# Kernel tuning notes

Hardware: AMD Instinct MI355X
Metric: run time of the kernel (lower is better)

Reference implementation:

```python
import jax, jax.numpy as jnp
import numpy as np

N_NODES = 10000
N_EDGES = 160000
IN_CH = 256
HIDDEN = 512
N_LAYERS = 2
W_SCALE = 0.05  # keep relu chain numerically tame


def setup_inputs() -> dict:
    key = jax.random.key(0)
    ks = jax.random.split(key, 8)
    x = jax.random.normal(ks[0], (N_NODES, IN_CH), dtype=jnp.float32)
    edge_index = jax.random.randint(ks[1], (2, N_EDGES), 0, N_NODES, dtype=jnp.int64)
    W_in = jax.random.normal(ks[2], (IN_CH, HIDDEN), dtype=jnp.float32) * W_SCALE
    b_in = jnp.zeros((HIDDEN,), jnp.float32)
    msg_W = jax.random.normal(ks[3], (N_LAYERS, HIDDEN, HIDDEN), dtype=jnp.float32) * W_SCALE
    msg_b = jnp.zeros((N_LAYERS, HIDDEN), jnp.float32)
    upd_W = jax.random.normal(ks[4], (N_LAYERS, 2 * HIDDEN, HIDDEN), dtype=jnp.float32) * W_SCALE
    upd_b = jnp.zeros((N_LAYERS, HIDDEN), jnp.float32)
    W_out = jax.random.normal(ks[5], (HIDDEN, 1), dtype=jnp.float32) * W_SCALE
    b_out = jnp.zeros((1,), jnp.float32)
    return {"x": x, "edge_index": edge_index, "W_in": W_in, "b_in": b_in,
            "msg_W": msg_W, "msg_b": msg_b, "upd_W": upd_W, "upd_b": upd_b,
            "W_out": W_out, "b_out": b_out}


def reference(x, edge_index, W_in, b_in, msg_W, msg_b, upd_W, upd_b, W_out, b_out):
    src = edge_index[0]  # x_j source nodes (PyG source_to_target flow)
    dst = edge_index[1]  # aggregate into destination nodes
    n = x.shape[0]
    h = jax.nn.relu(x @ W_in + b_in)  # [N, H]
    for l in range(msg_W.shape[0]):
        # message: relu(Linear(x_j)) on gathered source features  [E, H]
        m = jax.nn.relu(h[src] @ msg_W[l] + msg_b[l])
        # aggr='add': scatter-add over destination nodes  [N, H]
        aggr = jax.ops.segment_sum(m, dst, num_segments=n)
        # update: relu(Linear(concat([x, aggr])))  [N, H]
        h = jax.nn.relu(jnp.concatenate([h, aggr], axis=-1) @ upd_W[l] + upd_b[l])
    out = h @ W_out + b_out  # [N, 1]
    return out.squeeze(-1)
```

## Files before the change

### kernel.cpp

```cpp
#include <hip/hip_runtime.h>


typedef _Float16 half8 __attribute__((ext_vector_type(8)));
typedef float float4v __attribute__((ext_vector_type(4)));

#define ASYNC_COPY16(gptr, lptr)                                              \
    __builtin_amdgcn_global_load_lds(                                         \
        (const __attribute__((address_space(1))) void*)(gptr),                \
        (__attribute__((address_space(3))) void*)(lptr), 16, 0, 0)


__device__ __forceinline__ void gemm_body(int id,
    const _Float16* __restrict__ A1, int KT1,
    const _Float16* __restrict__ A2, int KT2,
    const _Float16* __restrict__ Wt, int KTw, int ktw2,
    const float* __restrict__ bias, _Float16* __restrict__ C,
    int M, int Mtiles, int packC, int do_relu,
    const float* __restrict__ Wout, const float* __restrict__ bout,
    float* __restrict__ outp)
{
    __shared__ _Float16 As[4096];
    __shared__ _Float16 Bs[4096];

    const int tid  = threadIdx.x;
    const int wave = tid >> 6, lane = tid & 63;

    const int cxcd = id & 7, j = id >> 3;
    const int mt = cxcd + 8 * (j >> 3);
    if (mt >= Mtiles) return;
    const int pn = j & 7;
    const int bm = mt * 64, bn = pn * 64;

    const int wr = (wave >> 1) * 32, wc = (wave & 1) * 32;
    const int m16 = lane & 15, quad = lane >> 4;

    float4v acc[2][2] = {};
    float bv[2];
    #pragma unroll
    for (int jj = 0; jj < 2; ++jj) bv[jj] = bias[bn + wc + jj * 16 + m16];

    for (int pass = 0; pass < 2; ++pass) {
        const _Float16* __restrict__ A = pass ? A2 : A1;
        if (A == nullptr) continue;
        const int KTa  = pass ? KT2 : KT1;
        const int ktw0 = pass ? ktw2 : 0;

        for (int kt = 0; kt < KTa; ++kt) {
            const _Float16* Ab = A  + (size_t)(mt * KTa + kt) * 4096;
            const _Float16* Wb = Wt + (size_t)(pn * KTw + ktw0 + kt) * 4096;
            #pragma unroll
            for (int t = 0; t < 2; ++t) {
                const int q = t * 4 + wave;
                ASYNC_COPY16(Ab + q * 512 + lane * 8, (char*)As + q * 1024);
                ASYNC_COPY16(Wb + q * 512 + lane * 8, (char*)Bs + q * 1024);
            }
            __syncthreads();
            #pragma unroll
            for (int c = 0; c < 2; ++c) {
                half8 af[2], bf[2];
                #pragma unroll
                for (int i2 = 0; i2 < 2; ++i2)
                    af[i2] = *(const half8*)
                        &As[((c * 4 + quad) * 64 + wr + i2 * 16 + m16) * 8];
                #pragma unroll
                for (int j2 = 0; j2 < 2; ++j2)
                    bf[j2] = *(const half8*)
                        &Bs[((c * 4 + quad) * 64 + wc + j2 * 16 + m16) * 8];
                #pragma unroll
                for (int i2 = 0; i2 < 2; ++i2)
                    #pragma unroll
                    for (int j2 = 0; j2 < 2; ++j2)
                        acc[i2][j2] = __builtin_amdgcn_mfma_f32_16x16x32_f16(
                            af[i2], bf[j2], acc[i2][j2], 0, 0, 0);
            }
            __syncthreads();
        }
    }

    if (outp) {
        #pragma unroll
        for (int i = 0; i < 2; ++i)
            #pragma unroll
            for (int rg = 0; rg < 4; ++rg) {
                const int r2 = wr + i * 16 + quad * 4 + rg;
                const int row = bm + r2;
                float pr = 0.f;
                #pragma unroll
                for (int j2 = 0; j2 < 2; ++j2) {
                    float v = fmaxf(acc[i][j2][rg] + bv[j2], 0.f);
                    pr += v * Wout[bn + wc + j2 * 16 + m16];
                }
                pr += __shfl_xor(pr, 1);
                pr += __shfl_xor(pr, 2);
                pr += __shfl_xor(pr, 4);
                pr += __shfl_xor(pr, 8);
                if (m16 == 0 && row < M)
                    atomicAdd(&outp[row],
                              pr + ((pn == 0 && wc == 0) ? bout[0] : 0.f));
            }
        return;
    }

    #pragma unroll
    for (int i = 0; i < 2; ++i)
        #pragma unroll
        for (int rg = 0; rg < 4; ++rg) {
            const int r2 = wr + i * 16 + quad * 4 + rg;
            const int row = bm + r2;
            if (row >= M) continue;
            #pragma unroll
            for (int j2 = 0; j2 < 2; ++j2) {
                float v = acc[i][j2][rg] + bv[j2];
                if (do_relu) v = fmaxf(v, 0.f);
                const int coff = wc + j2 * 16 + m16;
                if (packC) {
                    C[(size_t)((mt * 8 + pn) * 8 + (coff >> 3)) * 512
                      + r2 * 8 + (coff & 7)] = (_Float16)v;
                } else {
                    C[(size_t)row * 512 + bn + coff] = (_Float16)v;
                }
            }
        }
}

__global__ __launch_bounds__(256) void gemm_f16(
    const _Float16* __restrict__ A1, int KT1,
    const _Float16* __restrict__ A2, int KT2,
    const _Float16* __restrict__ Wt, int KTw, int ktw2,
    const float* __restrict__ bias, _Float16* __restrict__ C,
    int M, int Mtiles, int packC, int do_relu,
    const float* Wout, const float* bout, float* outp)
{
    gemm_body(blockIdx.x, A1, KT1, A2, KT2, Wt, KTw, ktw2,
              bias, C, M, Mtiles, packC, do_relu, Wout, bout, outp);
}

__device__ __forceinline__ void transpose_unit(
    const float* __restrict__ src, _Float16* __restrict__ dst, int R, int tb)
{
    const int rtiles = R >> 5;
    const int r0 = (tb % rtiles) * 32, c0 = (tb / rtiles) * 32;
    const int KT = R >> 6;
    __shared__ float t[32][33];
    const int tid = threadIdx.x;
    const int tx = tid & 31, ty = tid >> 5;
    #pragma unroll
    for (int i = 0; i < 32; i += 8)
        t[ty + i][tx] = src[(size_t)(r0 + ty + i) * 512 + c0 + tx];
    __syncthreads();
    if (tid < 128) {
        const int n  = c0 + (tid >> 2);
        const int k0 = r0 + (tid & 3) * 8;
        half8 o;
        #pragma unroll
        for (int j2 = 0; j2 < 8; ++j2)
            o[j2] = (_Float16)t[(tid & 3) * 8 + j2][tid >> 2];
        *(half8*)&dst[(size_t)(((n >> 6) * KT + (k0 >> 6)) * 8 + ((k0 >> 3) & 7)) * 512
                      + (n & 63) * 8] = o;
    }
}

__global__ __launch_bounds__(256) void fill_ingemm(
    const int* __restrict__ eidx, int* __restrict__ cursor,
    int* __restrict__ srcs, int E,
    const _Float16* __restrict__ xb, const _Float16* __restrict__ WinT,
    const float* __restrict__ b_in, _Float16* __restrict__ B0,
    int M, int Mtiles,
    const float* __restrict__ msg_W, _Float16* __restrict__ msgT,
    const float* __restrict__ upd_W, _Float16* __restrict__ updT)
{
    const int gemmU = ((Mtiles + 7) >> 3) * 64;
    const int fillU = (E + 255) >> 8;
    const int b = blockIdx.x;
    if (b < gemmU) {
        gemm_body(b, xb, 4, nullptr, 0, WinT, 4, 0,
                  b_in, B0, M, Mtiles, 1, 1, nullptr, nullptr, nullptr);
        return;
    }
    if (b < gemmU + fillU) {
        const int e = (b - gemmU) * 256 + threadIdx.x;
        if (e < E) {
            const int d = eidx[E + e];
            const int pos = atomicAdd(&cursor[d], 1);
            if (pos < 64) srcs[d * 64 + pos] = eidx[e];
        }
        return;
    }
    const int tB = b - gemmU - fillU;
    if (tB < 256)       transpose_unit(msg_W,              msgT,              512,  tB);
    else if (tB < 512)  transpose_unit(msg_W + 512 * 512,  msgT + 512 * 512,  512,  tB - 256);
    else if (tB < 1024) transpose_unit(upd_W,              updT,              1024, tB - 512);
    else                transpose_unit(upd_W + 1024 * 512, updT + 512 * 1024, 1024, tB - 1024);
}

__global__ __launch_bounds__(256) void prep(
    const float* __restrict__ W_in,  _Float16* __restrict__ WinT,
    const float* __restrict__ x,     _Float16* __restrict__ xb,
    int* __restrict__ cursor, float* __restrict__ outz,
    int n4, int M)
{
    const int b = blockIdx.x;
    const int tid = threadIdx.x;
    const int castU = (n4 + 255) >> 8;
    if (b < 128) {
        transpose_unit(W_in, WinT, 256, b);
    } else if (b < 128 + castU) {
        const int i = (b - 128) * 256 + tid;
        if (i < n4) {
            const float4 v = *(const float4*)(x + (size_t)i * 4);
            ushort4 s;
            union { _Float16 h; unsigned short u; } cv;
            cv.h = (_Float16)v.x; s.x = cv.u;
            cv.h = (_Float16)v.y; s.y = cv.u;
            cv.h = (_Float16)v.z; s.z = cv.u;
            cv.h = (_Float16)v.w; s.w = cv.u;
            const int f = i * 4;
            const int m = f >> 8, k = f & 255;
            *(ushort4*)((unsigned short*)xb
                + (size_t)(((m >> 6) * 4 + (k >> 6)) * 8 + ((k >> 3) & 7)) * 512
                + (m & 63) * 8 + (k & 7)) = s;
        }
    } else {
        const int zi = (b - 128 - castU) * 256 + tid;
        if (zi < M) { cursor[zi] = 0; outz[zi] = 0.f; }
    }
}

__global__ __launch_bounds__(256) void aggregate_f16(
    const _Float16* __restrict__ hmr, const int* __restrict__ cursor,
    const int* __restrict__ srcs, _Float16* __restrict__ ag, int n)
{
    const int l16  = threadIdx.x & 15;
    const int node = blockIdx.x * 16 + (threadIdx.x >> 4);
    if (node >= n) return;
    const int c8 = blockIdx.y * 128 + l16 * 8;
    const int beg = node * 64;
    const int end = beg + min(cursor[node], 64);
    float a[8] = {};
    int j = beg;
    for (; j + 3 < end; j += 4) {
        const half8 v0 = *(const half8*)(hmr + (size_t)srcs[j]     * 512 + c8);
        const half8 v1 = *(const half8*)(hmr + (size_t)srcs[j + 1] * 512 + c8);
        const half8 v2 = *(const half8*)(hmr + (size_t)srcs[j + 2] * 512 + c8);
        const half8 v3 = *(const half8*)(hmr + (size_t)srcs[j + 3] * 512 + c8);
        #pragma unroll
        for (int i = 0; i < 8; ++i)
            a[i] += ((float)v0[i] + (float)v1[i]) + ((float)v2[i] + (float)v3[i]);
    }
    for (; j < end; ++j) {
        const half8 v = *(const half8*)(hmr + (size_t)srcs[j] * 512 + c8);
        #pragma unroll
        for (int i = 0; i < 8; ++i) a[i] += (float)v[i];
    }
    half8 o;
    #pragma unroll
    for (int i = 0; i < 8; ++i) o[i] = (_Float16)a[i];
    *(half8*)(ag + (size_t)(((node >> 6) * 8 + (c8 >> 6)) * 8 + ((c8 >> 3) & 7)) * 512
              + (node & 63) * 8) = o;
}

extern "C" void kernel_launch(void* const* d_in, const int* in_sizes, int n_in,
                              void* d_out, int out_size, void* d_ws, size_t ws_size,
                              hipStream_t stream)
{
    const float* x     = (const float*)d_in[0];
    const int*   eidx  = (const int*)  d_in[1];
    const float* W_in  = (const float*)d_in[2];
    const float* b_in  = (const float*)d_in[3];
    const float* msg_W = (const float*)d_in[4];
    const float* msg_b = (const float*)d_in[5];
    const float* upd_W = (const float*)d_in[6];
    const float* upd_b = (const float*)d_in[7];
    const float* W_out = (const float*)d_in[8];
    const float* b_out = (const float*)d_in[9];

    const int IN = 256, H = 512;
    const int M = in_sizes[0] / IN;
    const int E = in_sizes[1] / 2;
    const int Mtiles = (M + 63) / 64;
    const size_t Mt64 = (size_t)Mtiles * 64;

    _Float16* xb   = (_Float16*)d_ws;
    _Float16* B0   = xb + Mt64 * IN;
    _Float16* B1   = B0 + Mt64 * H;
    _Float16* B2   = B1 + Mt64 * H;
    _Float16* WinT = B2 + Mt64 * H;
    _Float16* msgT = WinT + (size_t)H * IN;
    _Float16* updT = msgT + (size_t)2 * H * H;
    int* cursor = (int*)(updT + (size_t)2 * H * 2 * H);
    int* srcs   = cursor + M;

    const dim3 blk(256);
    const int gemmBlocks = ((Mtiles + 7) / 8) * 64;
    const dim3 aggrGrid((M + 15) / 16, 4);

    const int n4 = M * IN / 4;
    const int castU = (n4 + 255) / 256;
    const int fillU = (E + 255) / 256;
    const int zeroU = (M + 255) / 256;
    const int transU = 1536;

    prep<<<dim3(128 + castU + zeroU), blk, 0, stream>>>(
        W_in, WinT, x, xb, cursor, (float*)d_out, n4, M);
    fill_ingemm<<<dim3(gemmBlocks + fillU + transU), blk, 0, stream>>>(
        eidx, cursor, srcs, E, xb, WinT, b_in, B0, M, Mtiles,
        msg_W, msgT, upd_W, updT);

    gemm_f16<<<dim3(gemmBlocks), blk, 0, stream>>>(B0, 8, nullptr, 0,
        msgT, 8, 0, msg_b, B1, M, Mtiles, 0, 1,
        nullptr, nullptr, nullptr);
    aggregate_f16<<<aggrGrid, blk, 0, stream>>>(B1, cursor, srcs, B2, M);
    gemm_f16<<<dim3(gemmBlocks), blk, 0, stream>>>(B0, 8, B2, 8,
        updT, 16, 8, upd_b, B1, M, Mtiles, 1, 1,
        nullptr, nullptr, nullptr);
    gemm_f16<<<dim3(gemmBlocks), blk, 0, stream>>>(B1, 8, nullptr, 0,
        msgT + 512 * 512, 8, 0, msg_b + 512, B0, M, Mtiles, 0, 1,
        nullptr, nullptr, nullptr);
    aggregate_f16<<<aggrGrid, blk, 0, stream>>>(B0, cursor, srcs, B2, M);
    gemm_f16<<<dim3(gemmBlocks), blk, 0, stream>>>(B1, 8, B2, 8,
        updT + 512 * 1024, 16, 8, upd_b + 512, nullptr, M, Mtiles, 1, 1,
        W_out, b_out, (float*)d_out);
}
```

Measured before the change: 204.7 us.

## Split update GEMM into h-part fused with message GEMM and aggr-part

The update GEMM over concat([h, aggr]) is split into two halves. The h half runs in the same launch as the message GEMM (double grid) and writes an fp32 partial to a new buffer. After aggregation, the second GEMM handles only the aggr half and adds that partial back in. This moves half the update work off the serial path behind aggregation and fills more CUs in the message launch. The cost is an extra fp32 write and read of an N×512 partial buffer, plus more scattered epilogue reads.

```diff
diff --git a/kernel.cpp b/kernel.cpp
--- a/kernel.cpp
+++ b/kernel.cpp
@@ -11,11 +11,11 @@
 
 
 __device__ __forceinline__ void gemm_body(int id,
-    const _Float16* __restrict__ A1, int KT1,
-    const _Float16* __restrict__ A2, int KT2,
-    const _Float16* __restrict__ Wt, int KTw, int ktw2,
+    const _Float16* __restrict__ A, int KTa,
+    const _Float16* __restrict__ Wt, int KTw, int ktw0,
     const float* __restrict__ bias, _Float16* __restrict__ C,
-    int M, int Mtiles, int packC, int do_relu,
+    const float* __restrict__ Padd, float* __restrict__ Pout,
+    int M, int Mtiles, int mode,
     const float* __restrict__ Wout, const float* __restrict__ bout,
     float* __restrict__ outp)
 {
@@ -35,60 +35,58 @@
     const int m16 = lane & 15, quad = lane >> 4;
 
     float4v acc[2][2] = {};
-    float bv[2];
-    #pragma unroll
-    for (int jj = 0; jj < 2; ++jj) bv[jj] = bias[bn + wc + jj * 16 + m16];
-
-    for (int pass = 0; pass < 2; ++pass) {
-        const _Float16* __restrict__ A = pass ? A2 : A1;
-        if (A == nullptr) continue;
-        const int KTa  = pass ? KT2 : KT1;
-        const int ktw0 = pass ? ktw2 : 0;
-
-        for (int kt = 0; kt < KTa; ++kt) {
-            const _Float16* Ab = A  + (size_t)(mt * KTa + kt) * 4096;
-            const _Float16* Wb = Wt + (size_t)(pn * KTw + ktw0 + kt) * 4096;
+    float bv[2] = {0.f, 0.f};
+    if (bias) {
+        #pragma unroll
+        for (int jj = 0; jj < 2; ++jj) bv[jj] = bias[bn + wc + jj * 16 + m16];
+    }
+
+    for (int kt = 0; kt < KTa; ++kt) {
+        const _Float16* Ab = A  + (size_t)(mt * KTa + kt) * 4096;
+        const _Float16* Wb = Wt + (size_t)(pn * KTw + ktw0 + kt) * 4096;
+        #pragma unroll
+        for (int t = 0; t < 2; ++t) {
+            const int q = t * 4 + wave;
+            ASYNC_COPY16(Ab + q * 512 + lane * 8, (char*)As + q * 1024);
+            ASYNC_COPY16(Wb + q * 512 + lane * 8, (char*)Bs + q * 1024);
+        }
+        __syncthreads();
+        #pragma unroll
+        for (int c = 0; c < 2; ++c) {
+            half8 af[2], bf[2];
             #pragma unroll
-            for (int t = 0; t < 2; ++t) {
-                const int q = t * 4 + wave;
-                ASYNC_COPY16(Ab + q * 512 + lane * 8, (char*)As + q * 1024);
-                ASYNC_COPY16(Wb + q * 512 + lane * 8, (char*)Bs + q * 1024);
-            }
-            __syncthreads();
+            for (int i2 = 0; i2 < 2; ++i2)
+                af[i2] = *(const half8*)
+                    &As[((c * 4 + quad) * 64 + wr + i2 * 16 + m16) * 8];
             #pragma unroll
-            for (int c = 0; c < 2; ++c) {
-                half8 af[2], bf[2];
-                #pragma unroll
-                for (int i2 = 0; i2 < 2; ++i2)
-                    af[i2] = *(const half8*)
-                        &As[((c * 4 + quad) * 64 + wr + i2 * 16 + m16) * 8];
+            for (int j2 = 0; j2 < 2; ++j2)
+                bf[j2] = *(const half8*)
+                    &Bs[((c * 4 + quad) * 64 + wc + j2 * 16 + m16) * 8];
+            #pragma unroll
+            for (int i2 = 0; i2 < 2; ++i2)
                 #pragma unroll
                 for (int j2 = 0; j2 < 2; ++j2)
-                    bf[j2] = *(const half8*)
-                        &Bs[((c * 4 + quad) * 64 + wc + j2 * 16 + m16) * 8];
-                #pragma unroll
-                for (int i2 = 0; i2 < 2; ++i2)
-                    #pragma unroll
-                    for (int j2 = 0; j2 < 2; ++j2)
-                        acc[i2][j2] = __builtin_amdgcn_mfma_f32_16x16x32_f16(
-                            af[i2], bf[j2], acc[i2][j2], 0, 0, 0);
-            }
-            __syncthreads();
-        }
-    }
-
-    if (outp) {
-        #pragma unroll
-        for (int i = 0; i < 2; ++i)
-            #pragma unroll
-            for (int rg = 0; rg < 4; ++rg) {
-                const int r2 = wr + i * 16 + quad * 4 + rg;
-                const int row = bm + r2;
+                    acc[i2][j2] = __builtin_amdgcn_mfma_f32_16x16x32_f16(
+                        af[i2], bf[j2], acc[i2][j2], 0, 0, 0);
+        }
+        __syncthreads();
+    }
+
+    #pragma unroll
+    for (int i = 0; i < 2; ++i)
+        #pragma unroll
+        for (int rg = 0; rg < 4; ++rg) {
+            const int r2 = wr + i * 16 + quad * 4 + rg;
+            const int row = bm + r2;
+            if (mode == 4) {
                 float pr = 0.f;
                 #pragma unroll
                 for (int j2 = 0; j2 < 2; ++j2) {
-                    float v = fmaxf(acc[i][j2][rg] + bv[j2], 0.f);
-                    pr += v * Wout[bn + wc + j2 * 16 + m16];
+                    const int coff = wc + j2 * 16 + m16;
+                    float v = acc[i][j2][rg]
+                            + (row < M ? Padd[(size_t)row * 512 + bn + coff] : 0.f);
+                    v = fmaxf(v, 0.f);
+                    pr += v * Wout[bn + coff];
                 }
                 pr += __shfl_xor(pr, 1);
                 pr += __shfl_xor(pr, 2);
@@ -97,42 +95,53 @@
                 if (m16 == 0 && row < M)
                     atomicAdd(&outp[row],
                               pr + ((pn == 0 && wc == 0) ? bout[0] : 0.f));
+                continue;
             }
-        return;
-    }
-
-    #pragma unroll
-    for (int i = 0; i < 2; ++i)
-        #pragma unroll
-        for (int rg = 0; rg < 4; ++rg) {
-            const int r2 = wr + i * 16 + quad * 4 + rg;
-            const int row = bm + r2;
             if (row >= M) continue;
             #pragma unroll
             for (int j2 = 0; j2 < 2; ++j2) {
+                const int coff = wc + j2 * 16 + m16;
                 float v = acc[i][j2][rg] + bv[j2];
-                if (do_relu) v = fmaxf(v, 0.f);
-                const int coff = wc + j2 * 16 + m16;
-                if (packC) {
-                    C[(size_t)((mt * 8 + pn) * 8 + (coff >> 3)) * 512
-                      + r2 * 8 + (coff & 7)] = (_Float16)v;
+                if (mode == 3) v += Padd[(size_t)row * 512 + bn + coff];
+                if (mode == 2) {
+                    Pout[(size_t)row * 512 + bn + coff] = v;
                 } else {
-                    C[(size_t)row * 512 + bn + coff] = (_Float16)v;
+                    v = fmaxf(v, 0.f);
+                    if (mode == 0 || mode == 3) {
+                        C[(size_t)((mt * 8 + pn) * 8 + (coff >> 3)) * 512
+                          + r2 * 8 + (coff & 7)] = (_Float16)v;
+                    } else {
+                        C[(size_t)row * 512 + bn + coff] = (_Float16)v;
+                    }
                 }
             }
         }
 }
 
-__global__ __launch_bounds__(256) void gemm_f16(
-    const _Float16* __restrict__ A1, int KT1,
-    const _Float16* __restrict__ A2, int KT2,
-    const _Float16* __restrict__ Wt, int KTw, int ktw2,
-    const float* __restrict__ bias, _Float16* __restrict__ C,
-    int M, int Mtiles, int packC, int do_relu,
+__global__ __launch_bounds__(256) void msg_updA(
+    const _Float16* __restrict__ h,
+    const _Float16* __restrict__ msgT_l, const float* __restrict__ msg_b_l,
+    _Float16* __restrict__ Z,
+    const _Float16* __restrict__ updT_l, const float* __restrict__ upd_b_l,
+    float* __restrict__ P, int M, int Mtiles)
+{
+    const int gemmU = ((Mtiles + 7) >> 3) * 64;
+    if ((int)blockIdx.x < gemmU)
+        gemm_body(blockIdx.x, h, 8, msgT_l, 8, 0, msg_b_l, Z,
+                  nullptr, nullptr, M, Mtiles, 1, nullptr, nullptr, nullptr);
+    else
+        gemm_body(blockIdx.x - gemmU, h, 8, updT_l, 16, 0, upd_b_l, nullptr,
+                  nullptr, P, M, Mtiles, 2, nullptr, nullptr, nullptr);
+}
+
+__global__ __launch_bounds__(256) void updB(
+    const _Float16* __restrict__ aggr, const _Float16* __restrict__ updT_l,
+    const float* __restrict__ P, _Float16* __restrict__ C,
+    int M, int Mtiles, int mode,
     const float* Wout, const float* bout, float* outp)
 {
-    gemm_body(blockIdx.x, A1, KT1, A2, KT2, Wt, KTw, ktw2,
-              bias, C, M, Mtiles, packC, do_relu, Wout, bout, outp);
+    gemm_body(blockIdx.x, aggr, 8, updT_l, 16, 8, nullptr, C,
+              P, nullptr, M, Mtiles, mode, Wout, bout, outp);
 }
 
 __device__ __forceinline__ void transpose_unit(
@@ -173,8 +182,8 @@
     const int fillU = (E + 255) >> 8;
     const int b = blockIdx.x;
     if (b < gemmU) {
-        gemm_body(b, xb, 4, nullptr, 0, WinT, 4, 0,
-                  b_in, B0, M, Mtiles, 1, 1, nullptr, nullptr, nullptr);
+        gemm_body(b, xb, 4, WinT, 4, 0, b_in, B0,
+                  nullptr, nullptr, M, Mtiles, 0, nullptr, nullptr, nullptr);
         return;
     }
     if (b < gemmU + fillU) {
@@ -287,7 +296,8 @@
     _Float16* WinT = B2 + Mt64 * H;
     _Float16* msgT = WinT + (size_t)H * IN;
     _Float16* updT = msgT + (size_t)2 * H * H;
-    int* cursor = (int*)(updT + (size_t)2 * H * 2 * H);
+    float*    Pbuf = (float*)(updT + (size_t)2 * H * 2 * H);
+    int* cursor = (int*)(Pbuf + Mt64 * H);
     int* srcs   = cursor + M;
 
     const dim3 blk(256);
@@ -306,18 +316,17 @@
         eidx, cursor, srcs, E, xb, WinT, b_in, B0, M, Mtiles,
         msg_W, msgT, upd_W, updT);
 
-    gemm_f16<<<dim3(gemmBlocks), blk, 0, stream>>>(B0, 8, nullptr, 0,
-        msgT, 8, 0, msg_b, B1, M, Mtiles, 0, 1,
-        nullptr, nullptr, nullptr);
+    msg_updA<<<dim3(2 * gemmBlocks), blk, 0, stream>>>(
+        B0, msgT, msg_b, B1, updT, upd_b, Pbuf, M, Mtiles);
     aggregate_f16<<<aggrGrid, blk, 0, stream>>>(B1, cursor, srcs, B2, M);
-    gemm_f16<<<dim3(gemmBlocks), blk, 0, stream>>>(B0, 8, B2, 8,
-        updT, 16, 8, upd_b, B1, M, Mtiles, 1, 1,
-        nullptr, nullptr, nullptr);
-    gemm_f16<<<dim3(gemmBlocks), blk, 0, stream>>>(B1, 8, nullptr, 0,
-        msgT + 512 * 512, 8, 0, msg_b + 512, B0, M, Mtiles, 0, 1,
-        nullptr, nullptr, nullptr);
+    updB<<<dim3(gemmBlocks), blk, 0, stream>>>(
+        B2, updT, Pbuf, B1, M, Mtiles, 3, nullptr, nullptr, nullptr);
+
+    msg_updA<<<dim3(2 * gemmBlocks), blk, 0, stream>>>(
+        B1, msgT + 512 * 512, msg_b + 512, B0,
+        updT + 512 * 1024, upd_b + 512, Pbuf, M, Mtiles);
     aggregate_f16<<<aggrGrid, blk, 0, stream>>>(B0, cursor, srcs, B2, M);
-    gemm_f16<<<dim3(gemmBlocks), blk, 0, stream>>>(B1, 8, B2, 8,
-        updT + 512 * 1024, 16, 8, upd_b + 512, nullptr, M, Mtiles, 1, 1,
+    updB<<<dim3(gemmBlocks), blk, 0, stream>>>(
+        B2, updT + 512 * 1024, Pbuf, nullptr, M, Mtiles, 4,
         W_out, b_out, (float*)d_out);
 }
```

Measured after the change: 208.3 us. Within noise of the previous version (+1.7%).
